# Kernel optimization log

Measured on AMD Instinct MI355X. Metric: run time of the kernel, lower is better.

Reference implementation:

```python
import jax, jax.numpy as jnp
import numpy as np

B, T, H, K = 16, 2048, 512, 15
FIRE_TH = 1.0
SMOOTH = 1.0
NOISE_TH = 0.0
LN_EPS = 1e-5


def setup_inputs() -> dict:
    key = jax.random.key(0)
    ks = jax.random.split(key, 8)
    s = lambda n: 1.0 / np.sqrt(n)
    return {
        "x": jax.random.normal(ks[0], (B, T, H), jnp.float32),
        "x_lens": jax.random.randint(ks[1], (B,), T // 2, T + 1),
        "pw1_w": jax.random.normal(ks[2], (2 * H, H), jnp.float32) * s(H),
        "pw1_b": jnp.zeros((2 * H,), jnp.float32),
        "dw_w": jax.random.normal(ks[3], (H, K), jnp.float32) * s(K),
        "dw_b": jnp.zeros((H,), jnp.float32),
        "ln_g": jnp.ones((H,), jnp.float32),
        "ln_b": jnp.zeros((H,), jnp.float32),
        "pw2_w": jax.random.normal(ks[4], (H, H), jnp.float32) * s(H),
        "pw2_b": jnp.zeros((H,), jnp.float32),
        "lin_w": jax.random.normal(ks[5], (H,), jnp.float32) * s(H),
        "lin_b": jnp.zeros((), jnp.float32),
    }


def _layer_norm(x, g, b):
    m = x.mean(-1, keepdims=True)
    v = ((x - m) ** 2).mean(-1, keepdims=True)
    return (x - m) * jax.lax.rsqrt(v + LN_EPS) * g + b


def _swish(x):
    return x * jax.nn.sigmoid(x)


def _conv_module(x, pw1_w, pw1_b, dw_w, dw_b, ln_g, ln_b, pw2_w, pw2_b):
    # wenet ConvolutionModule (causal, layer_norm): pw-conv -> GLU -> causal depthwise -> LN -> swish -> pw-conv
    h = jnp.einsum('bth,oh->bto', x, pw1_w) + pw1_b          # (B,T,2H)
    h = h[..., :H] * jax.nn.sigmoid(h[..., H:])              # GLU over channel halves
    hp = jnp.pad(h, ((0, 0), (K - 1, 0), (0, 0)))            # causal left pad
    rhs = dw_w.T[:, None, :]                                 # (K, 1, H) depthwise kernel
    h = jax.lax.conv_general_dilated(
        hp, rhs, window_strides=(1,), padding='VALID',
        dimension_numbers=('NWC', 'WIO', 'NWC'),
        feature_group_count=H) + dw_b                        # (B,T,H)
    h = _swish(_layer_norm(h, ln_g, ln_b))
    return jnp.einsum('bth,oh->bto', h, pw2_w) + pw2_b


def _cif_scan(x, alphas):
    # sequential integrate-and-fire over time, batched over B
    def step(carry, inp):
        integrate, frame = carry
        alpha, xt = inp                                       # (B,), (B,H)
        dist = FIRE_TH - integrate
        integrate = integrate + alpha
        fire = integrate >= FIRE_TH
        cur = jnp.where(fire, dist, alpha)
        remain = alpha - cur
        frame_acc = frame + cur[:, None] * xt
        new_frame = jnp.where(fire[:, None], remain[:, None] * xt, frame_acc)
        new_int = jnp.where(fire, integrate - FIRE_TH, integrate)
        return (new_int, new_frame), (integrate, frame_acc)
    init = (jnp.zeros((B,), x.dtype), jnp.zeros((B, H), x.dtype))
    _, (fires, frames) = jax.lax.scan(step, init, (alphas.T, x.transpose(1, 0, 2)))
    return fires.T, frames.transpose(1, 0, 2)                 # (B,T), (B,T,H)


def _gather_fired(fires, frames):
    # ragged gather of fired frames into a fixed (B,T,H) padded buffer
    mask = fires >= FIRE_TH                                   # (B,T)
    dest = jnp.where(mask, jnp.cumsum(mask, axis=1) - 1, T)   # dump non-fired to slot T
    out = jnp.zeros((B, T + 1, H), frames.dtype)
    out = out.at[jnp.arange(B)[:, None], dest].set(frames)
    fired = out[:, :T]
    return fired, jnp.flip(fired, axis=-1)                    # torch.flip(dims=[1]) flips hidden dim


def reference(x, x_lens, pw1_w, pw1_b, dw_w, dw_b, ln_g, ln_b, pw2_w, pw2_b, lin_w, lin_b):
    mask = (jnp.arange(T)[None, :] < x_lens[:, None]).astype(x.dtype)   # (B,T)
    hidden = _conv_module(x, pw1_w, pw1_b, dw_w, dw_b, ln_g, ln_b, pw2_w, pw2_b)
    logits = jnp.einsum('bth,h->bt', hidden, lin_w) + lin_b
    alphas = jax.nn.relu(jax.nn.sigmoid(logits) * SMOOTH - NOISE_TH) * mask
    predicted_token_nums = alphas.sum(-1)
    fires, frames = _cif_scan(x, alphas)
    fired_frames, r_fired_frames = _gather_fired(fires, frames)
    return fired_frames, predicted_token_nums, r_fired_frames
```

## Files before the change

### kernel.cpp

```cpp
#include <hip/hip_runtime.h>
#include <math.h>

#define B_ 16
#define T_ 2048
#define H_ 512
#define K_ 15
#define M_ (B_*T_)

typedef __attribute__((ext_vector_type(8))) short short8;
typedef __attribute__((ext_vector_type(4))) float f32x4;

__device__ __forceinline__ unsigned short f2bf(float f) {
  union { float f; unsigned u; } v; v.f = f;
  unsigned r = v.u + 0x7FFFu + ((v.u >> 16) & 1u);
  return (unsigned short)(r >> 16);
}
__device__ __forceinline__ float bf2f(unsigned short b) {
  union { float f; unsigned u; } v; v.u = ((unsigned)b) << 16;
  return v.f;
}

__device__ __forceinline__ void async_load16(const void* g, void* l) {
  __builtin_amdgcn_global_load_lds((const __attribute__((address_space(1))) void*)g,
                                   (__attribute__((address_space(3))) void*)l, 16, 0, 0);
}

__global__ void convx_k(const float* __restrict__ x, unsigned short* __restrict__ hi,
                        unsigned short* __restrict__ lo, int n4) {
  int i = blockIdx.x * blockDim.x + threadIdx.x;
  int stride = gridDim.x * blockDim.x;
  for (; i < n4; i += stride) {
    float4 v = ((const float4*)x)[i];
    ushort4 h, l;
    h.x = f2bf(v.x); l.x = f2bf(v.x - bf2f(h.x));
    h.y = f2bf(v.y); l.y = f2bf(v.y - bf2f(h.y));
    h.z = f2bf(v.z); l.z = f2bf(v.z - bf2f(h.z));
    h.w = f2bf(v.w); l.w = f2bf(v.w - bf2f(h.w));
    ((ushort4*)hi)[i] = h;
    ((ushort4*)lo)[i] = l;
  }
}

__global__ __launch_bounds__(256) void weff_k(const float* __restrict__ pw2_w,
    const float* __restrict__ pw2_b, const float* __restrict__ lin_w,
    const float* __restrict__ lin_b, float* __restrict__ weff) {
  __shared__ float red[256];
  if (blockIdx.x < 8) {
    int h = blockIdx.x * 64 + (threadIdx.x & 63);
    int og = threadIdx.x >> 6;
    float acc = 0.f;
    for (int o = og * 128; o < og * 128 + 128; ++o) acc += pw2_w[o * H_ + h] * lin_w[o];
    red[threadIdx.x] = acc;
    __syncthreads();
    if (threadIdx.x < 64)
      weff[h] = red[threadIdx.x] + red[threadIdx.x + 64] + red[threadIdx.x + 128] + red[threadIdx.x + 192];
  } else {
    int i = threadIdx.x;
    red[i] = pw2_b[i] * lin_w[i] + pw2_b[i + 256] * lin_w[i + 256];
    __syncthreads();
    for (int s = 128; s > 0; s >>= 1) {
      if (i < s) red[i] += red[i + s];
      __syncthreads();
    }
    if (i == 0) weff[H_] = red[0] + lin_b[0];
  }
}

__global__ __launch_bounds__(256) void gemm_mfma_k(
    const unsigned short* __restrict__ Ahi, const unsigned short* __restrict__ Alo,
    const unsigned short* __restrict__ Whi, const unsigned short* __restrict__ Wlo,
    const float* __restrict__ bias, float* __restrict__ g) {
  __shared__ short Ah[2][128 * 32];
  __shared__ short Al[2][128 * 32];
  __shared__ short Bh[2][128 * 32];
  __shared__ short Bl[2][128 * 32];
  const int tid = threadIdx.x;
  const int m0 = blockIdx.x * 128;
  const int n0 = blockIdx.y * 64;
  const int w = tid >> 6, lane = tid & 63;
  const int wr = w >> 1, wc = w & 1;

  f32x4 acc[4][4];
#pragma unroll
  for (int mt = 0; mt < 4; ++mt)
#pragma unroll
    for (int nt = 0; nt < 4; ++nt) acc[mt][nt] = (f32x4){0.f, 0.f, 0.f, 0.f};

  int offA[2], offB[2], ldsb[2];
#pragma unroll
  for (int j = 0; j < 2; ++j) {
    int L = j * 256 + tid;
    int r = L >> 2;
    int csrc = (L & 3) ^ ((r >> 1) & 3);
    offA[j] = (m0 + r) * 512 + csrc * 8;
    int wrow = (r < 64) ? (n0 + r) : (n0 + 448 + r);
    offB[j] = wrow * 512 + csrc * 8;
    ldsb[j] = __builtin_amdgcn_readfirstlane((j * 256 + w * 64) * 16);
  }

  const int q = lane >> 4;
  int aAddr[4], bAddr[4];
#pragma unroll
  for (int mt = 0; mt < 4; ++mt) {
    int rA = wr * 64 + mt * 16 + (lane & 15);
    aAddr[mt] = rA * 64 + (q ^ ((rA >> 1) & 3)) * 16;
  }
#pragma unroll
  for (int nt = 0; nt < 4; ++nt) {
    int rB = (nt >> 1) * 64 + wc * 32 + (nt & 1) * 16 + (lane & 15);
    bAddr[nt] = rB * 64 + (q ^ ((rB >> 1) & 3)) * 16;
  }

#pragma unroll
  for (int j = 0; j < 2; ++j) {
    async_load16(Ahi + offA[j], (char*)Ah[0] + ldsb[j]);
    async_load16(Alo + offA[j], (char*)Al[0] + ldsb[j]);
    async_load16(Whi + offB[j], (char*)Bh[0] + ldsb[j]);
    async_load16(Wlo + offB[j], (char*)Bl[0] + ldsb[j]);
  }

#pragma unroll 2
  for (int kk = 0; kk < 16; ++kk) {
    const int cur = kk & 1;
    const int nxt = cur ^ 1;
    __syncthreads();

    short8 ah[4], al[4], bh[4], bl[4];
#pragma unroll
    for (int mt = 0; mt < 4; ++mt) {
      ah[mt] = *(const short8*)((const char*)Ah[cur] + aAddr[mt]);
      al[mt] = *(const short8*)((const char*)Al[cur] + aAddr[mt]);
    }
#pragma unroll
    for (int nt = 0; nt < 4; ++nt) {
      bh[nt] = *(const short8*)((const char*)Bh[cur] + bAddr[nt]);
      bl[nt] = *(const short8*)((const char*)Bl[cur] + bAddr[nt]);
    }

    if (kk < 15) {
      const int k0 = (kk + 1) * 32;
#pragma unroll
      for (int j = 0; j < 2; ++j) {
        async_load16(Ahi + offA[j] + k0, (char*)Ah[nxt] + ldsb[j]);
        async_load16(Alo + offA[j] + k0, (char*)Al[nxt] + ldsb[j]);
        async_load16(Whi + offB[j] + k0, (char*)Bh[nxt] + ldsb[j]);
        async_load16(Wlo + offB[j] + k0, (char*)Bl[nxt] + ldsb[j]);
      }
    }
    __builtin_amdgcn_sched_barrier(0);

#pragma unroll
    for (int mt = 0; mt < 4; ++mt)
#pragma unroll
      for (int nt = 0; nt < 4; ++nt) {
        acc[mt][nt] = __builtin_amdgcn_mfma_f32_16x16x32_bf16(ah[mt], bh[nt], acc[mt][nt], 0, 0, 0);
        acc[mt][nt] = __builtin_amdgcn_mfma_f32_16x16x32_bf16(al[mt], bh[nt], acc[mt][nt], 0, 0, 0);
        acc[mt][nt] = __builtin_amdgcn_mfma_f32_16x16x32_bf16(ah[mt], bl[nt], acc[mt][nt], 0, 0, 0);
      }
  }

  const int col = lane & 15, rq = lane >> 4;
#pragma unroll
  for (int mt = 0; mt < 4; ++mt) {
#pragma unroll
    for (int ntp = 0; ntp < 2; ++ntp) {
      int gcol = n0 + wc * 32 + ntp * 16 + col;
      float ba = bias[gcol];
      float bg = bias[512 + gcol];
#pragma unroll
      for (int r = 0; r < 4; ++r) {
        int m = m0 + wr * 64 + mt * 16 + rq * 4 + r;
        float a = acc[mt][ntp][r] + ba;
        float gt = acc[mt][2 + ntp][r] + bg;
        g[(size_t)m * 512 + gcol] = a / (1.f + expf(-gt));
      }
    }
  }
}

__global__ __launch_bounds__(512) void conv_ln_k(const float* __restrict__ g,
    const float* __restrict__ dw_w, const float* __restrict__ dw_b,
    const float* __restrict__ ln_g, const float* __restrict__ ln_b,
    const float* __restrict__ weff, const int* __restrict__ x_lens,
    float* __restrict__ aT) {
  __shared__ float wlds[H_ * K_];
  __shared__ float tbuf[16][512];
  __shared__ float mvs[16], rss[16];
  const int tid = threadIdx.x;
  const int c = tid;
  const int t0 = blockIdx.x * 64;
  const int b = blockIdx.y;

  for (int i = tid; i < H_ * K_; i += 512) wlds[i] = dw_w[i];
  const int xlen = x_lens[b];
  const float* gb = g + ((size_t)b * T_) * H_ + c;

  float gwin[30];
#pragma unroll
  for (int i = 0; i < 30; ++i) {
    int t = t0 - 14 + i;
    gwin[i] = (t >= 0) ? gb[(size_t)t * H_] : 0.f;
  }
  __syncthreads();
  float wreg[15];
#pragma unroll
  for (int k = 0; k < 15; ++k) wreg[k] = wlds[c * 15 + k];
  const float dwb = dw_b[c], lg = ln_g[c], lb = ln_b[c], we = weff[c];
  const float beff = weff[H_];
  const int tt = tid >> 5, p = tid & 31;

#pragma unroll 1
  for (int qc = 0; qc < 4; ++qc) {
    float h2[16];
#pragma unroll
    for (int j = 0; j < 16; ++j) {
      float s = dwb;
#pragma unroll
      for (int k = 0; k < 15; ++k) s += gwin[j + k] * wreg[k];
      h2[j] = s;
      tbuf[j][c] = s;
    }
    __syncthreads();
    float s1 = 0.f, s2 = 0.f;
#pragma unroll
    for (int k = 0; k < 16; ++k) {
      float v = tbuf[tt][k * 32 + p];
      s1 += v; s2 += v * v;
    }
#pragma unroll
    for (int off = 16; off > 0; off >>= 1) {
      s1 += __shfl_down(s1, off, 32);
      s2 += __shfl_down(s2, off, 32);
    }
    if (p == 0) {
      float m = s1 * (1.f / 512.f);
      float v = s2 * (1.f / 512.f) - m * m;
      mvs[tt] = m;
      rss[tt] = rsqrtf(v + 1e-5f);
    }
    __syncthreads();
#pragma unroll
    for (int j = 0; j < 16; ++j) {
      float y = (h2[j] - mvs[j]) * rss[j] * lg + lb;
      float sw = y / (1.f + expf(-y));
      tbuf[j][c] = sw * we;
    }
    __syncthreads();
    float s = 0.f;
#pragma unroll
    for (int k = 0; k < 16; ++k) s += tbuf[tt][k * 32 + p];
#pragma unroll
    for (int off = 16; off > 0; off >>= 1) s += __shfl_down(s, off, 32);
    if (p == 0) {
      float logit = s + beff;
      float a = 1.f / (1.f + expf(-logit));
      int t = t0 + qc * 16 + tt;
      if (t >= xlen) a = 0.f;
      aT[t * B_ + b] = a;
    }
    if (qc < 3) {
#pragma unroll
      for (int i = 0; i < 14; ++i) gwin[i] = gwin[i + 16];
#pragma unroll
      for (int i = 0; i < 16; ++i)
        gwin[14 + i] = gb[(size_t)(t0 + qc * 16 + 16 + i) * H_];
    }
    __syncthreads();
  }
}

__global__ __launch_bounds__(64) void cif_p1_k(const float* __restrict__ aT,
                                               float* __restrict__ chk) {
  const int b = threadIdx.x;
  if (b >= B_) return;
  const float* ar = aT + b;
  float integ = 0.f;
  float bufA[32], bufB[32];
#pragma unroll
  for (int j = 0; j < 32; ++j) bufA[j] = ar[j * B_];
#pragma unroll 1
  for (int s = 0; s < 64; s += 2) {
#pragma unroll
    for (int j = 0; j < 32; ++j) bufB[j] = ar[((s + 1) * 32 + j) * B_];
    chk[s * B_ + b] = integ;
#pragma unroll
    for (int j = 0; j < 32; ++j) {
      float ni = integ + bufA[j];
      integ = ni - floorf(ni);
    }
    if (s + 2 < 64) {
#pragma unroll
      for (int j = 0; j < 32; ++j) bufA[j] = ar[((s + 2) * 32 + j) * B_];
    }
    chk[(s + 1) * B_ + b] = integ;
#pragma unroll
    for (int j = 0; j < 32; ++j) {
      float ni = integ + bufB[j];
      integ = ni - floorf(ni);
    }
  }
}

__global__ __launch_bounds__(64) void cif_p2_k(const float* __restrict__ aT,
    const float* __restrict__ chk, float* __restrict__ wdT, float* __restrict__ wrT,
    int* __restrict__ fire_pos, int* __restrict__ nfires, float* __restrict__ tok) {
  const int b = blockIdx.x;
  const int seg = threadIdx.x;
  const int t0 = seg * 32;
  float integ = chk[seg * B_ + b];
  float a[32];
#pragma unroll
  for (int j = 0; j < 32; ++j) a[j] = aT[(t0 + j) * B_ + b];
  unsigned fmask = 0u;
  float ssum = 0.f;
#pragma unroll
  for (int j = 0; j < 32; ++j) {
    float al = a[j];
    float dist = 1.0f - integ;
    float ni = integ + al;
    bool fire = ni >= 1.0f;
    float cur = fire ? dist : al;
    wdT[(t0 + j) * B_ + b] = cur;
    wrT[(t0 + j) * B_ + b] = al - cur;
    if (fire) fmask |= (1u << j);
    integ = ni - floorf(ni);
    ssum += al;
  }
  const int cnt = __popc(fmask);
  int incl = cnt;
#pragma unroll
  for (int off = 1; off < 64; off <<= 1) {
    int v = __shfl_up(incl, off, 64);
    if (seg >= off) incl += v;
  }
  int idx = incl - cnt;
  unsigned m = fmask;
  while (m) {
    int j = __ffs(m) - 1;
    m &= m - 1;
    fire_pos[b * T_ + idx++] = t0 + j;
  }
  if (seg == 63) nfires[b] = incl;
#pragma unroll
  for (int off = 32; off > 0; off >>= 1) ssum += __shfl_down(ssum, off, 64);
  if (seg == 0) tok[b] = ssum;
}

__global__ __launch_bounds__(128) void frames_k(const float* __restrict__ x,
    const float* __restrict__ aT, const float* __restrict__ wdT,
    const float* __restrict__ wrT, const int* __restrict__ fire_pos,
    const int* __restrict__ nfires, float* __restrict__ out0, float* __restrict__ out2) {
  const int b = blockIdx.y;
  const int j = blockIdx.x;
  const int h = threadIdx.x << 2;
  const size_t ob = ((size_t)b * T_ + j) * H_;
  if (j >= nfires[b]) {
    float4 z = make_float4(0.f, 0.f, 0.f, 0.f);
    *(float4*)(out0 + ob + h) = z;
    *(float4*)(out2 + ob + h) = z;
    return;
  }
  const int te = fire_pos[b * T_ + j];
  const int ts = (j > 0) ? fire_pos[b * T_ + j - 1] : -1;
  const float* xb = x + ((size_t)b * T_) * H_;
  float4 acc = make_float4(0.f, 0.f, 0.f, 0.f);
  if (j > 0) {
    float w = wrT[ts * B_ + b];
    float4 xv = *(const float4*)(xb + (size_t)ts * H_ + h);
    acc.x = w * xv.x; acc.y = w * xv.y; acc.z = w * xv.z; acc.w = w * xv.w;
  }
  for (int t = ts + 1; t < te; ++t) {
    float w = aT[t * B_ + b];
    float4 xv = *(const float4*)(xb + (size_t)t * H_ + h);
    acc.x += w * xv.x; acc.y += w * xv.y; acc.z += w * xv.z; acc.w += w * xv.w;
  }
  {
    float w = wdT[te * B_ + b];
    float4 xv = *(const float4*)(xb + (size_t)te * H_ + h);
    acc.x += w * xv.x; acc.y += w * xv.y; acc.z += w * xv.z; acc.w += w * xv.w;
  }
  *(float4*)(out0 + ob + h) = acc;
  float4 racc = make_float4(acc.w, acc.z, acc.y, acc.x);
  *(float4*)(out2 + ob + (H_ - 4 - h)) = racc;
}

extern "C" void kernel_launch(void* const* d_in, const int* in_sizes, int n_in,
                              void* d_out, int out_size, void* d_ws, size_t ws_size,
                              hipStream_t stream) {
  const float* x     = (const float*)d_in[0];
  const int*   xlens = (const int*)d_in[1];
  const float* pw1_w = (const float*)d_in[2];
  const float* pw1_b = (const float*)d_in[3];
  const float* dw_w  = (const float*)d_in[4];
  const float* dw_b  = (const float*)d_in[5];
  const float* ln_g  = (const float*)d_in[6];
  const float* ln_b  = (const float*)d_in[7];
  const float* pw2_w = (const float*)d_in[8];
  const float* pw2_b = (const float*)d_in[9];
  const float* lin_w = (const float*)d_in[10];
  const float* lin_b = (const float*)d_in[11];

  float* out0 = (float*)d_out;
  float* tok  = out0 + (size_t)B_ * T_ * H_;
  float* out2 = tok + B_;

  char* ws = (char*)d_ws;
  float* g             = (float*)ws;
  unsigned short* Ahi  = (unsigned short*)(ws + (size_t)M_ * H_ * 4);
  unsigned short* Alo  = Ahi + (size_t)M_ * H_;
  unsigned short* Whi  = Alo + (size_t)M_ * H_;
  unsigned short* Wlo  = Whi + (size_t)2 * H_ * H_;
  float* aT       = (float*)(Wlo + (size_t)2 * H_ * H_);
  float* wdT      = aT + B_ * T_;
  float* wrT      = wdT + B_ * T_;
  int*   fire_pos = (int*)(wrT + B_ * T_);
  int*   nfires   = fire_pos + B_ * T_;
  float* weff     = (float*)(nfires + 64);
  float* chk      = weff + 1024;

  convx_k<<<2048, 256, 0, stream>>>(x, Ahi, Alo, M_ * H_ / 4);
  convx_k<<<256, 256, 0, stream>>>(pw1_w, Whi, Wlo, 2 * H_ * H_ / 4);
  weff_k<<<9, 256, 0, stream>>>(pw2_w, pw2_b, lin_w, lin_b, weff);
  gemm_mfma_k<<<dim3(256, 8), 256, 0, stream>>>(Ahi, Alo, Whi, Wlo, pw1_b, g);
  conv_ln_k<<<dim3(32, 16), 512, 0, stream>>>(g, dw_w, dw_b, ln_g, ln_b, weff, xlens, aT);
  cif_p1_k<<<1, 64, 0, stream>>>(aT, chk);
  cif_p2_k<<<16, 64, 0, stream>>>(aT, chk, wdT, wrT, fire_pos, nfires, tok);
  frames_k<<<dim3(2048, 16), 128, 0, stream>>>(x, aT, wdT, wrT, fire_pos, nfires, out0, out2);
}
```

Before: 452.7 us.

## Remap GEMM blocks per XCD and split-barrier pipeline the K loop

```diff
diff --git a/kernel.cpp b/kernel.cpp
--- a/kernel.cpp
+++ b/kernel.cpp
@@ -75,8 +75,10 @@
   __shared__ short Bh[2][128 * 32];
   __shared__ short Bl[2][128 * 32];
   const int tid = threadIdx.x;
-  const int m0 = blockIdx.x * 128;
-  const int n0 = blockIdx.y * 64;
+  const int bid = blockIdx.x;
+  const int xcd = bid & 7, ii = bid >> 3;
+  const int m0 = (((xcd << 5) + (ii >> 3))) * 128;
+  const int n0 = (ii & 7) * 64;
   const int w = tid >> 6, lane = tid & 63;
   const int wr = w >> 1, wc = w & 1;
 
@@ -115,40 +117,52 @@
   for (int j = 0; j < 2; ++j) {
     async_load16(Ahi + offA[j], (char*)Ah[0] + ldsb[j]);
     async_load16(Alo + offA[j], (char*)Al[0] + ldsb[j]);
+  }
+#pragma unroll
+  for (int j = 0; j < 2; ++j) {
     async_load16(Whi + offB[j], (char*)Bh[0] + ldsb[j]);
     async_load16(Wlo + offB[j], (char*)Bl[0] + ldsb[j]);
   }
 
+  short8 ah[4], al[4], bh[4], bl[4];
+
 #pragma unroll 2
-  for (int kk = 0; kk < 16; ++kk) {
+  for (int kk = 0; kk < 15; ++kk) {
     const int cur = kk & 1;
     const int nxt = cur ^ 1;
-    __syncthreads();
-
-    short8 ah[4], al[4], bh[4], bl[4];
+    const int k1 = (kk + 1) * 32;
+
+    __builtin_amdgcn_sched_barrier(0);
+    asm volatile("s_waitcnt vmcnt(4)" ::: "memory");
+    __builtin_amdgcn_s_barrier();
+    __builtin_amdgcn_sched_barrier(0);
 #pragma unroll
     for (int mt = 0; mt < 4; ++mt) {
       ah[mt] = *(const short8*)((const char*)Ah[cur] + aAddr[mt]);
       al[mt] = *(const short8*)((const char*)Al[cur] + aAddr[mt]);
     }
 #pragma unroll
+    for (int j = 0; j < 2; ++j) {
+      async_load16(Ahi + offA[j] + k1, (char*)Ah[nxt] + ldsb[j]);
+      async_load16(Alo + offA[j] + k1, (char*)Al[nxt] + ldsb[j]);
+    }
+
+    __builtin_amdgcn_sched_barrier(0);
+    asm volatile("s_waitcnt vmcnt(4)" ::: "memory");
+    __builtin_amdgcn_s_barrier();
+    __builtin_amdgcn_sched_barrier(0);
+#pragma unroll
     for (int nt = 0; nt < 4; ++nt) {
       bh[nt] = *(const short8*)((const char*)Bh[cur] + bAddr[nt]);
       bl[nt] = *(const short8*)((const char*)Bl[cur] + bAddr[nt]);
     }
-
-    if (kk < 15) {
-      const int k0 = (kk + 1) * 32;
-#pragma unroll
-      for (int j = 0; j < 2; ++j) {
-        async_load16(Ahi + offA[j] + k0, (char*)Ah[nxt] + ldsb[j]);
-        async_load16(Alo + offA[j] + k0, (char*)Al[nxt] + ldsb[j]);
-        async_load16(Whi + offB[j] + k0, (char*)Bh[nxt] + ldsb[j]);
-        async_load16(Wlo + offB[j] + k0, (char*)Bl[nxt] + ldsb[j]);
-      }
-    }
-    __builtin_amdgcn_sched_barrier(0);
-
+#pragma unroll
+    for (int j = 0; j < 2; ++j) {
+      async_load16(Whi + offB[j] + k1, (char*)Bh[nxt] + ldsb[j]);
+      async_load16(Wlo + offB[j] + k1, (char*)Bl[nxt] + ldsb[j]);
+    }
+
+    __builtin_amdgcn_s_setprio(1);
 #pragma unroll
     for (int mt = 0; mt < 4; ++mt)
 #pragma unroll
@@ -157,6 +171,38 @@
         acc[mt][nt] = __builtin_amdgcn_mfma_f32_16x16x32_bf16(al[mt], bh[nt], acc[mt][nt], 0, 0, 0);
         acc[mt][nt] = __builtin_amdgcn_mfma_f32_16x16x32_bf16(ah[mt], bl[nt], acc[mt][nt], 0, 0, 0);
       }
+    __builtin_amdgcn_s_setprio(0);
+  }
+
+  {
+    __builtin_amdgcn_sched_barrier(0);
+    asm volatile("s_waitcnt vmcnt(4)" ::: "memory");
+    __builtin_amdgcn_s_barrier();
+    __builtin_amdgcn_sched_barrier(0);
+#pragma unroll
+    for (int mt = 0; mt < 4; ++mt) {
+      ah[mt] = *(const short8*)((const char*)Ah[1] + aAddr[mt]);
+      al[mt] = *(const short8*)((const char*)Al[1] + aAddr[mt]);
+    }
+    __builtin_amdgcn_sched_barrier(0);
+    asm volatile("s_waitcnt vmcnt(0)" ::: "memory");
+    __builtin_amdgcn_s_barrier();
+    __builtin_amdgcn_sched_barrier(0);
+#pragma unroll
+    for (int nt = 0; nt < 4; ++nt) {
+      bh[nt] = *(const short8*)((const char*)Bh[1] + bAddr[nt]);
+      bl[nt] = *(const short8*)((const char*)Bl[1] + bAddr[nt]);
+    }
+    __builtin_amdgcn_s_setprio(1);
+#pragma unroll
+    for (int mt = 0; mt < 4; ++mt)
+#pragma unroll
+      for (int nt = 0; nt < 4; ++nt) {
+        acc[mt][nt] = __builtin_amdgcn_mfma_f32_16x16x32_bf16(ah[mt], bh[nt], acc[mt][nt], 0, 0, 0);
+        acc[mt][nt] = __builtin_amdgcn_mfma_f32_16x16x32_bf16(al[mt], bh[nt], acc[mt][nt], 0, 0, 0);
+        acc[mt][nt] = __builtin_amdgcn_mfma_f32_16x16x32_bf16(ah[mt], bl[nt], acc[mt][nt], 0, 0, 0);
+      }
+    __builtin_amdgcn_s_setprio(0);
   }
 
   const int col = lane & 15, rq = lane >> 4;
@@ -421,7 +467,7 @@
   convx_k<<<2048, 256, 0, stream>>>(x, Ahi, Alo, M_ * H_ / 4);
   convx_k<<<256, 256, 0, stream>>>(pw1_w, Whi, Wlo, 2 * H_ * H_ / 4);
   weff_k<<<9, 256, 0, stream>>>(pw2_w, pw2_b, lin_w, lin_b, weff);
-  gemm_mfma_k<<<dim3(256, 8), 256, 0, stream>>>(Ahi, Alo, Whi, Wlo, pw1_b, g);
+  gemm_mfma_k<<<2048, 256, 0, stream>>>(Ahi, Alo, Whi, Wlo, pw1_b, g);
   conv_ln_k<<<dim3(32, 16), 512, 0, stream>>>(g, dw_w, dw_b, ln_g, ln_b, weff, xlens, aT);
   cif_p1_k<<<1, 64, 0, stream>>>(aT, chk);
   cif_p2_k<<<16, 64, 0, stream>>>(aT, chk, wdT, wrT, fire_pos, nfires, tok);
```

New measurement: 442.8 us. -2.2%, faster.

## Triple-buffer A tiles with explicit vmcnt waits and XCD-aware block remap

Applied to the files above, without the earlier changes.

```diff
diff --git a/kernel.cpp b/kernel.cpp
--- a/kernel.cpp
+++ b/kernel.cpp
@@ -70,13 +70,15 @@
     const unsigned short* __restrict__ Ahi, const unsigned short* __restrict__ Alo,
     const unsigned short* __restrict__ Whi, const unsigned short* __restrict__ Wlo,
     const float* __restrict__ bias, float* __restrict__ g) {
-  __shared__ short Ah[2][128 * 32];
-  __shared__ short Al[2][128 * 32];
+  __shared__ short Ah[3][128 * 32];
+  __shared__ short Al[3][128 * 32];
   __shared__ short Bh[2][128 * 32];
   __shared__ short Bl[2][128 * 32];
   const int tid = threadIdx.x;
-  const int m0 = blockIdx.x * 128;
-  const int n0 = blockIdx.y * 64;
+  const int bid = blockIdx.x;
+  const int xcd = bid & 7, ii = bid >> 3;
+  const int m0 = (((xcd << 5) + (ii >> 3))) * 128;
+  const int n0 = (ii & 7) * 64;
   const int w = tid >> 6, lane = tid & 63;
   const int wr = w >> 1, wc = w & 1;
 
@@ -115,40 +117,64 @@
   for (int j = 0; j < 2; ++j) {
     async_load16(Ahi + offA[j], (char*)Ah[0] + ldsb[j]);
     async_load16(Alo + offA[j], (char*)Al[0] + ldsb[j]);
+  }
+#pragma unroll
+  for (int j = 0; j < 2; ++j) {
     async_load16(Whi + offB[j], (char*)Bh[0] + ldsb[j]);
     async_load16(Wlo + offB[j], (char*)Bl[0] + ldsb[j]);
   }
-
-#pragma unroll 2
+#pragma unroll
+  for (int j = 0; j < 2; ++j) {
+    async_load16(Ahi + offA[j] + 32, (char*)Ah[1] + ldsb[j]);
+    async_load16(Alo + offA[j] + 32, (char*)Al[1] + ldsb[j]);
+  }
+
+  short8 ah[4], al[4], bh[4], bl[4];
+
+#pragma unroll
   for (int kk = 0; kk < 16; ++kk) {
-    const int cur = kk & 1;
-    const int nxt = cur ^ 1;
-    __syncthreads();
-
-    short8 ah[4], al[4], bh[4], bl[4];
+    const int ca = kk % 3;
+    const int cb = kk & 1;
+
+    __builtin_amdgcn_sched_barrier(0);
+    if (kk == 15) {
+      asm volatile("s_waitcnt vmcnt(0)" ::: "memory");
+    } else {
+      asm volatile("s_waitcnt vmcnt(4)" ::: "memory");
+    }
+    __builtin_amdgcn_s_barrier();
+    __builtin_amdgcn_sched_barrier(0);
+
 #pragma unroll
     for (int mt = 0; mt < 4; ++mt) {
-      ah[mt] = *(const short8*)((const char*)Ah[cur] + aAddr[mt]);
-      al[mt] = *(const short8*)((const char*)Al[cur] + aAddr[mt]);
+      ah[mt] = *(const short8*)((const char*)Ah[ca] + aAddr[mt]);
+      al[mt] = *(const short8*)((const char*)Al[ca] + aAddr[mt]);
     }
 #pragma unroll
     for (int nt = 0; nt < 4; ++nt) {
-      bh[nt] = *(const short8*)((const char*)Bh[cur] + bAddr[nt]);
-      bl[nt] = *(const short8*)((const char*)Bl[cur] + bAddr[nt]);
+      bh[nt] = *(const short8*)((const char*)Bh[cb] + bAddr[nt]);
+      bl[nt] = *(const short8*)((const char*)Bl[cb] + bAddr[nt]);
     }
 
     if (kk < 15) {
-      const int k0 = (kk + 1) * 32;
+      const int kB = (kk + 1) * 32, sb = (kk + 1) & 1;
 #pragma unroll
       for (int j = 0; j < 2; ++j) {
-        async_load16(Ahi + offA[j] + k0, (char*)Ah[nxt] + ldsb[j]);
-        async_load16(Alo + offA[j] + k0, (char*)Al[nxt] + ldsb[j]);
-        async_load16(Whi + offB[j] + k0, (char*)Bh[nxt] + ldsb[j]);
-        async_load16(Wlo + offB[j] + k0, (char*)Bl[nxt] + ldsb[j]);
+        async_load16(Whi + offB[j] + kB, (char*)Bh[sb] + ldsb[j]);
+        async_load16(Wlo + offB[j] + kB, (char*)Bl[sb] + ldsb[j]);
       }
     }
+    if (kk < 14) {
+      const int kA = (kk + 2) * 32, sa = (kk + 2) % 3;
+#pragma unroll
+      for (int j = 0; j < 2; ++j) {
+        async_load16(Ahi + offA[j] + kA, (char*)Ah[sa] + ldsb[j]);
+        async_load16(Alo + offA[j] + kA, (char*)Al[sa] + ldsb[j]);
+      }
+    }
     __builtin_amdgcn_sched_barrier(0);
 
+    __builtin_amdgcn_s_setprio(1);
 #pragma unroll
     for (int mt = 0; mt < 4; ++mt)
 #pragma unroll
@@ -157,6 +183,7 @@
         acc[mt][nt] = __builtin_amdgcn_mfma_f32_16x16x32_bf16(al[mt], bh[nt], acc[mt][nt], 0, 0, 0);
         acc[mt][nt] = __builtin_amdgcn_mfma_f32_16x16x32_bf16(ah[mt], bl[nt], acc[mt][nt], 0, 0, 0);
       }
+    __builtin_amdgcn_s_setprio(0);
   }
 
   const int col = lane & 15, rq = lane >> 4;
@@ -421,7 +448,7 @@
   convx_k<<<2048, 256, 0, stream>>>(x, Ahi, Alo, M_ * H_ / 4);
   convx_k<<<256, 256, 0, stream>>>(pw1_w, Whi, Wlo, 2 * H_ * H_ / 4);
   weff_k<<<9, 256, 0, stream>>>(pw2_w, pw2_b, lin_w, lin_b, weff);
-  gemm_mfma_k<<<dim3(256, 8), 256, 0, stream>>>(Ahi, Alo, Whi, Wlo, pw1_b, g);
+  gemm_mfma_k<<<2048, 256, 0, stream>>>(Ahi, Alo, Whi, Wlo, pw1_b, g);
   conv_ln_k<<<dim3(32, 16), 512, 0, stream>>>(g, dw_w, dw_b, ln_g, ln_b, weff, xlens, aT);
   cif_p1_k<<<1, 64, 0, stream>>>(aT, chk);
   cif_p2_k<<<16, 64, 0, stream>>>(aT, chk, wdT, wrT, fire_pos, nfires, tok);
```

Result: no change. 449.2 us (-0.8%).
